# Optimization experiments

Hardware: AMD Instinct MI355X
Metric: run time of the kernel (lower is better)

## Reference

```python
import jax, jax.numpy as jnp
import numpy as np

ALPHA = 0.5
TEMPORAL_UNIT = 0
B, T, D = 8, 1024, 320
TIME_MAX = 10_000_000


def setup_inputs() -> dict:
    key = jax.random.key(0)
    k1, k2, k3 = jax.random.split(key, 3)
    z1 = jax.random.normal(k1, (B, T, D), dtype=jnp.float32)
    z2 = jax.random.normal(k2, (B, T, D), dtype=jnp.float32)
    event_time = jnp.sort(
        jax.random.randint(k3, (B, T), 0, TIME_MAX, dtype=jnp.int32), axis=-1
    )
    return {"z1": z1, "z2": z2, "event_time": event_time}


def _neg_logsoftmax_offdiag(sim):
    # tril(sim,-1)[...,:-1] + triu(sim,1)[...,1:]  -> (.., N, N-1), then -log_softmax
    logits = jnp.tril(sim, -1)[..., :-1] + jnp.triu(sim, 1)[..., 1:]
    return -jax.nn.log_softmax(logits, axis=-1)


def _instance_loss(z1, z2):
    b, t = z1.shape[0], z1.shape[1]
    if b == 1:
        return jnp.float32(0.0)
    z = jnp.concatenate([z1, z2], axis=0).transpose(1, 0, 2)  # (T, 2B, D)
    sim = jnp.einsum('tid,tjd->tij', z, z)                    # (T, 2B, 2B)
    logits = _neg_logsoftmax_offdiag(sim)                     # (T, 2B, 2B-1)
    i = jnp.arange(b)
    return (logits[:, i, b + i - 1].mean() + logits[:, b + i, i].mean()) / 2


def _temporal_loss(z1, z2):
    t = z1.shape[1]
    if t == 1:
        return jnp.float32(0.0)
    z = jnp.concatenate([z1, z2], axis=1)                     # (B, 2T, D)
    sim = jnp.einsum('bid,bjd->bij', z, z)                    # (B, 2T, 2T)
    logits = _neg_logsoftmax_offdiag(sim)                     # (B, 2T, 2T-1)
    ti = jnp.arange(t)
    return (logits[:, ti, t + ti - 1].mean() + logits[:, t + ti, ti].mean()) / 2


def _pool_and_filter(z, time):
    # max_pool1d(kernel=2, stride=1) over time axis
    bsz, seq_len, dim = z.shape
    pooled = jnp.maximum(z[:, :-1], z[:, 1:])                  # (B, T-1, D)
    pooled_time = (time[:, :-1] + time[:, 1:]) // 2            # (B, T-1)
    deltas = jnp.diff(time, axis=-1)                           # (B, T-1)
    indices = jnp.argsort(deltas, axis=-1)                     # permutation of 0..T-2
    mask = indices < seq_len // 2                              # exactly T//2 Trues/row
    tm1 = seq_len - 1
    ar = jnp.arange(tm1)
    # stable in-order selection of masked positions: masked keys keep their index,
    # unmasked keys are pushed past the end; sort + take first T//2
    sel = jnp.sort(jnp.where(mask, ar, ar + tm1), axis=-1)[:, : seq_len // 2]
    pooled = jnp.take_along_axis(pooled, sel[:, :, None], axis=1)
    pooled_time = jnp.take_along_axis(pooled_time, sel, axis=1)
    return pooled, pooled_time


def _hier_loss(z1, z2, time, alpha=ALPHA, temporal_unit=TEMPORAL_UNIT):
    loss = jnp.float32(0.0)
    d = 0
    while z1.shape[1] > 1:  # static Python loop over hierarchy levels
        if alpha != 0:
            loss = loss + alpha * _instance_loss(z1, z2)
        if d >= temporal_unit and (1 - alpha) != 0:
            loss = loss + (1 - alpha) * _temporal_loss(z1, z2)
        d += 1
        z1, _ = _pool_and_filter(z1, time)
        z2, time = _pool_and_filter(z2, time)
    if z1.shape[1] == 1:
        if alpha != 0:
            loss = loss + alpha * _instance_loss(z1, z2)
        d += 1
    return loss / d


def reference(z1, z2, event_time):
    return _hier_loss(z1, z2, event_time)
```

## Files before the change

### kernel.cpp

```cpp
#include <hip/hip_runtime.h>
#include <cstdint>
#include <cstddef>

#define D_DIM 320
#define NEGINF (-1e30f)

typedef __attribute__((ext_vector_type(8))) short bf16x8_t;
typedef __attribute__((ext_vector_type(4))) float f32x4_t;
typedef __attribute__((ext_vector_type(16))) float f32x16_t;

struct Tab {
  int T[11], S[11], zoff[11], wsoff[11];
  int tileStart[12], instStart[12], rstart[12];
  float scale[11];
  int totTemp, totInst, totr;
};

__device__ __forceinline__ float bf2f(unsigned short u) {
  union { unsigned int i; float f; } v; v.i = ((unsigned int)u) << 16; return v.f;
}
__device__ __forceinline__ unsigned short f2bf(float f) {
  union { float f; unsigned int i; } u; u.f = f;
  unsigned int b = u.i + 0x7FFFu + ((u.i >> 16) & 1u);
  return (unsigned short)(b >> 16);
}

__device__ __forceinline__ const unsigned short* zrowb(
    const unsigned short* __restrict__ z1, const unsigned short* __restrict__ z2,
    int b, int T, int r) {
  return (r < T) ? (z1 + ((size_t)b * T + r) * D_DIM)
                 : (z2 + ((size_t)b * T + (r - T)) * D_DIM);
}

#define GLOAD_LDS16(SRC, DST)                                                   \
  __builtin_amdgcn_global_load_lds(                                             \
      (const __attribute__((address_space(1))) void*)(SRC),                     \
      (__attribute__((address_space(3))) void*)(DST), 16, 0, 0)

#define BUF1 8192
#define BUF2 16384

#define STAGE(koff, bufofs)                                                     \
    do {                                                                        \
      GLOAD_LDS16(gA0 + (koff), dA0 + (bufofs));                                \
      GLOAD_LDS16(gA1 + (koff), dA1 + (bufofs));                                \
      GLOAD_LDS16(gB0 + (koff), dB0 + (bufofs));                                \
      GLOAD_LDS16(gB1 + (koff), dB1 + (bufofs));                                \
    } while (0)

#define PHASE3(k, bo, bo2, VM, DO_PF)                                           \
    do {                                                                        \
      asm volatile("s_waitcnt vmcnt(" #VM ")" ::: "memory");                    \
      __builtin_amdgcn_s_barrier();                                             \
      if (DO_PF) STAGE((k + 2) * 32, bo2);                                      \
      bf16x8_t af[4], bfr[4];                                                   \
      _Pragma("unroll")                                                         \
      for (int at = 0; at < 4; ++at)                                            \
        af[at] = *(const bf16x8_t*)(vA + (bo) + at * 128);                      \
      _Pragma("unroll")                                                         \
      for (int ct = 0; ct < 4; ++ct)                                            \
        bfr[ct] = *(const bf16x8_t*)(vB + (bo) + ct * 128);                     \
      asm volatile("s_waitcnt lgkmcnt(0)" ::: "memory");                        \
      __builtin_amdgcn_sched_barrier(0);                                        \
      __builtin_amdgcn_s_setprio(1);                                            \
      _Pragma("unroll")                                                         \
      for (int ct = 0; ct < 4; ++ct)                                            \
        _Pragma("unroll")                                                       \
        for (int at = 0; at < 4; ++at)                                          \
          acc[at][ct] = __builtin_amdgcn_mfma_f32_16x16x32_bf16(                \
              af[at], bfr[ct], acc[at][ct], 0, 0, 0);                           \
      __builtin_amdgcn_s_setprio(0);                                            \
    } while (0)

__device__ __forceinline__ void tile_body(
    unsigned char* smem, int tid,
    const unsigned short* zz1, const unsigned short* zz2,
    int b, int T, int S, int rb, int sg,
    float* wm, float* wv, float* wp) {
  int N = 2 * T;
  int row0 = rb * 128, col0 = sg * 128;
  int w = tid >> 6, lane = tid & 63;
  int lq = lane >> 4, lr = lane & 15;
  int wr = w >> 1, wc = w & 1;

  unsigned short* lds = (unsigned short*)smem;

  int ra0 = row0 + lane;        if (ra0 > N - 1) ra0 = N - 1;
  int ra1 = row0 + 64 + lane;   if (ra1 > N - 1) ra1 = N - 1;
  int ca0 = col0 + lane;        if (ca0 > N - 1) ca0 = N - 1;
  int ca1 = col0 + 64 + lane;   if (ca1 > N - 1) ca1 = N - 1;
  const unsigned short* gA0 = zrowb(zz1, zz2, b, T, ra0) + w * 8;
  const unsigned short* gA1 = zrowb(zz1, zz2, b, T, ra1) + w * 8;
  const unsigned short* gB0 = zrowb(zz1, zz2, b, T, ca0) + w * 8;
  const unsigned short* gB1 = zrowb(zz1, zz2, b, T, ca1) + w * 8;
  unsigned short* dA0 = &lds[((w) * 128 + lane) * 8];
  unsigned short* dA1 = &lds[((w) * 128 + 64 + lane) * 8];
  unsigned short* dB0 = &lds[((4 + w) * 128 + lane) * 8];
  unsigned short* dB1 = &lds[((4 + w) * 128 + 64 + lane) * 8];

  f32x4_t acc[4][4];
#pragma unroll
  for (int at = 0; at < 4; ++at)
#pragma unroll
    for (int ct = 0; ct < 4; ++ct) acc[at][ct] = (f32x4_t)(0.f);

  const unsigned short* vA = &lds[((lq) * 128 + wr * 64 + lr) * 8];
  const unsigned short* vB = &lds[((4 + lq) * 128 + wc * 64 + lr) * 8];

  STAGE(0, 0);
  STAGE(32, BUF1);
  PHASE3(0, 0,    BUF2, 4, 1);
  PHASE3(1, BUF1, 0,    4, 1);
  PHASE3(2, BUF2, BUF1, 4, 1);
  PHASE3(3, 0,    BUF2, 4, 1);
  PHASE3(4, BUF1, 0,    4, 1);
  PHASE3(5, BUF2, BUF1, 4, 1);
  PHASE3(6, 0,    BUF2, 4, 1);
  PHASE3(7, BUF1, 0,    4, 1);
  PHASE3(8, BUF2, 0,    4, 0);
  PHASE3(9, 0,    0,    0, 0);
  __builtin_amdgcn_s_barrier();

  float (*mS)[128] = (float(*)[128])(smem);
  float (*sS)[128] = (float(*)[128])(smem + 1024);
  float (*mC)[128] = (float(*)[128])(smem + 2048);
  float (*sC)[128] = (float(*)[128])(smem + 3072);

#pragma unroll
  for (int at = 0; at < 4; ++at) {
#pragma unroll
    for (int rg = 0; rg < 4; ++rg) {
      int rloc = wr * 64 + at * 16 + lq * 4 + rg;
      int rglob = row0 + rloc;
      int posr = (rglob < T) ? rglob + T : rglob - T;
      float v[4];
#pragma unroll
      for (int ct = 0; ct < 4; ++ct) {
        int cg = col0 + wc * 64 + ct * 16 + lr;
        float val = acc[at][ct][rg];
        if (rglob < N && cg == posr) {
          wp[b * N + rglob] = val;
          wp[b * N + cg] = val;
        }
        v[ct] = (cg < N && cg != rglob) ? val : NEGINF;
      }
      float m = fmaxf(fmaxf(v[0], v[1]), fmaxf(v[2], v[3]));
#pragma unroll
      for (int o = 1; o < 16; o <<= 1) m = fmaxf(m, __shfl_xor(m, o));
      float sv = __expf(v[0] - m) + __expf(v[1] - m) +
                 __expf(v[2] - m) + __expf(v[3] - m);
#pragma unroll
      for (int o = 1; o < 16; o <<= 1) sv += __shfl_xor(sv, o);
      if (lr == 0) { mS[wc][rloc] = m; sS[wc][rloc] = sv; }
    }
  }
  if (rb != sg) {
#pragma unroll
    for (int ct = 0; ct < 4; ++ct) {
      float m = NEGINF;
#pragma unroll
      for (int at = 0; at < 4; ++at)
#pragma unroll
        for (int rg = 0; rg < 4; ++rg) m = fmaxf(m, acc[at][ct][rg]);
      m = fmaxf(m, __shfl_xor(m, 16));
      m = fmaxf(m, __shfl_xor(m, 32));
      float s = 0.f;
#pragma unroll
      for (int at = 0; at < 4; ++at)
#pragma unroll
        for (int rg = 0; rg < 4; ++rg) s += __expf(acc[at][ct][rg] - m);
      s += __shfl_xor(s, 16);
      s += __shfl_xor(s, 32);
      if (lq == 0) {
        mC[wr][wc * 64 + ct * 16 + lr] = m;
        sC[wr][wc * 64 + ct * 16 + lr] = s;
      }
    }
  }
  __syncthreads();

  if (tid < 128) {
    int rglob = row0 + tid;
    if (rglob < N) {
      float m0 = mS[0][tid], m1 = mS[1][tid];
      float m = fmaxf(m0, m1);
      float sv = sS[0][tid] * __expf(m0 - m) + sS[1][tid] * __expf(m1 - m);
      int idx = (b * S + sg) * N + rglob;
      wm[idx] = m;
      wv[idx] = sv;
    }
    if (rb != sg) {
      float m0 = mC[0][tid], m1 = mC[1][tid];
      float m = fmaxf(m0, m1);
      float sv = sC[0][tid] * __expf(m0 - m) + sC[1][tid] * __expf(m1 - m);
      int idx = (b * S + rb) * N + col0 + tid;
      wm[idx] = m;
      wv[idx] = sv;
    }
  }
}

__device__ __forceinline__ float inst_wave(
    const unsigned short* zz1, const unsigned short* zz2, int T, int t, int lane) {
  int lq = lane >> 4, lr = lane & 15;
  const unsigned short* zr = (lr < 8)
      ? zz1 + ((size_t)lr * T + t) * D_DIM
      : zz2 + ((size_t)(lr - 8) * T + t) * D_DIM;
  zr += lq * 8;
  f32x4_t c = (f32x4_t)(0.f);
#pragma unroll
  for (int k = 0; k < 10; ++k) {
    bf16x8_t a = *(const bf16x8_t*)(zr + k * 32);
    c = __builtin_amdgcn_mfma_f32_16x16x32_bf16(a, a, c, 0, 0, 0);
  }
  float lsum = 0.f;
#pragma unroll
  for (int rg = 0; rg < 4; ++rg) {
    int rrow = lq * 4 + rg;
    float v = c[rg];
    float x = (lr != rrow) ? v : NEGINF;
    float m = x;
#pragma unroll
    for (int o = 1; o < 16; o <<= 1) m = fmaxf(m, __shfl_xor(m, o));
    float s = __expf(x - m);
#pragma unroll
    for (int o = 1; o < 16; o <<= 1) s += __shfl_xor(s, o);
    int pos = (rrow < 8) ? rrow + 8 : rrow - 8;
    if (lr == pos) lsum += m + __logf(s) - v;
  }
#pragma unroll
  for (int o = 1; o < 64; o <<= 1) lsum += __shfl_xor(lsum, o);
  return lsum;
}

__global__ __launch_bounds__(256) void convert_kernel(
    const float* __restrict__ i1, const float* __restrict__ i2,
    unsigned short* __restrict__ o1, unsigned short* __restrict__ o2,
    int n4, float* __restrict__ out, int outn) {
  int i = blockIdx.x * 256 + threadIdx.x;
  if (i < outn) out[i] = 0.f;
  int stride = gridDim.x * 256;
  for (int j = i; j < n4; j += stride) {
    float4 v = ((const float4*)i1)[j];
    ushort4 r;
    r.x = f2bf(v.x); r.y = f2bf(v.y); r.z = f2bf(v.z); r.w = f2bf(v.w);
    ((ushort4*)o1)[j] = r;
    float4 u = ((const float4*)i2)[j];
    ushort4 q;
    q.x = f2bf(u.x); q.y = f2bf(u.y); q.z = f2bf(u.z); q.w = f2bf(u.w);
    ((ushort4*)o2)[j] = q;
  }
}

__global__ __launch_bounds__(256, 3) void work0_kernel(
    const int* __restrict__ time0,
    const unsigned short* __restrict__ z1, const unsigned short* __restrict__ z2,
    float* __restrict__ wsm, float* __restrict__ wss, float* __restrict__ wpos,
    float* __restrict__ wsInst,
    int* __restrict__ SET0, int* __restrict__ L0LEN,
    int* __restrict__ SET5, int* __restrict__ L5LEN) {
  __shared__ __align__(16) unsigned char smem[49152];
  int bx = blockIdx.x;
  int tid = threadIdx.x;

  if (bx < 8) {
    int b = bx;
    int lane = tid & 63, wid = tid >> 6;
    int* tcur = (int*)smem;
    unsigned* hist = (unsigned*)(smem + 4096);
    unsigned short* cum = (unsigned short*)(smem + 12288);
    unsigned long long* arr = (unsigned long long*)(smem + 16384);
    int* sortedIdx = (int*)(smem + 24576);
    int* tnew = (int*)(smem + 28672);
    int* srcK = (int*)(smem + 30720);
    int* setA = (int*)(smem + 32768);
    int* setB = (int*)(smem + 36864);
    int* lenA = (int*)(smem + 40960);
    int* lenB = (int*)(smem + 45056);
    unsigned* minW = (unsigned*)(smem + 47104);
    unsigned* maxW = (unsigned*)(smem + 47168);
    unsigned* wsum = (unsigned*)(smem + 47232);
    int* wcnt = (int*)(smem + 47296);

#pragma unroll
    for (int i = 0; i < 4; ++i) {
      int e = tid + 256 * i;
      tcur[e] = time0[b * 1024 + e];
      setA[e] = e;
      lenA[e] = 1;
    }
    __syncthreads();

    int pp = 0;
    for (int lvl = 1; lvl <= 10; ++lvl) {
      int T = 2048 >> lvl;
      int n = T - 1, half = T >> 1;
      bool act[4];
      int dd[4];
      unsigned bkey[4];
      unsigned mn = 0xFFFFFFFFu, mx = 0u;
#pragma unroll
      for (int i = 0; i < 4; ++i) {
        int e = tid + 256 * i;
        act[i] = e < n;
        dd[i] = 0; bkey[i] = 0;
        if (act[i]) {
          dd[i] = tcur[e + 1] - tcur[e];
          bkey[i] = __float_as_uint((float)dd[i]);
          mn = mn < bkey[i] ? mn : bkey[i];
          mx = mx > bkey[i] ? mx : bkey[i];
        }
        hist[e] = 0;
        hist[e + 1024] = 0;
      }
#pragma unroll
      for (int o = 1; o < 64; o <<= 1) {
        unsigned m2 = (unsigned)__shfl_xor((int)mn, o);
        unsigned x2 = (unsigned)__shfl_xor((int)mx, o);
        mn = mn < m2 ? mn : m2;
        mx = mx > x2 ? mx : x2;
      }
      if (lane == 0) { minW[wid] = mn; maxW[wid] = mx; }
      __syncthreads();

      unsigned bmin = 0xFFFFFFFFu, bmax = 0;
#pragma unroll
      for (int i = 0; i < 4; ++i) {
        bmin = bmin < minW[i] ? bmin : minW[i];
        bmax = bmax > maxW[i] ? bmax : maxW[i];
      }
      unsigned long long range = (unsigned long long)(bmax - bmin) + 1;
      unsigned long long scl = (2048ULL << 30) / range;
      int bkt[4]; unsigned av[4];
#pragma unroll
      for (int i = 0; i < 4; ++i) {
        if (act[i]) {
          int bk = (int)(((unsigned long long)(bkey[i] - bmin) * scl) >> 30);
          bkt[i] = bk > 2047 ? 2047 : bk;
          av[i] = atomicAdd(&hist[bkt[i]], 1u);
        }
      }
      __syncthreads();

      {
        unsigned lv[8];
        unsigned s = 0;
#pragma unroll
        for (int j = 0; j < 8; ++j) { lv[j] = hist[8 * tid + j]; s += lv[j]; }
        unsigned inc = s;
#pragma unroll
        for (int o = 1; o < 64; o <<= 1) {
          unsigned t = (unsigned)__shfl_up((int)inc, o);
          if (lane >= o) inc += t;
        }
        if (lane == 63) wsum[wid] = inc;
        __syncthreads();
        unsigned wpre = 0;
        for (int j = 0; j < wid; ++j) wpre += wsum[j];
        unsigned ex = wpre + inc - s;
#pragma unroll
        for (int j = 0; j < 8; ++j) { cum[8 * tid + j] = (unsigned short)ex; ex += lv[j]; }
      }
      __syncthreads();

      unsigned long long key[4];
      int base[4], occ[4];
#pragma unroll
      for (int i = 0; i < 4; ++i) {
        base[i] = 0; occ[i] = 0;
        if (act[i]) {
          key[i] = ((unsigned long long)(unsigned)dd[i] << 10) |
                   (unsigned)(tid + 256 * i);
          base[i] = (int)cum[bkt[i]];
          arr[base[i] + av[i]] = key[i];
        }
      }
      __syncthreads();

      int cnt[4] = {0, 0, 0, 0};
      int mocc = 0;
#pragma unroll
      for (int i = 0; i < 4; ++i) {
        if (act[i]) {
          occ[i] = (int)hist[bkt[i]];
          mocc = occ[i] > mocc ? occ[i] : mocc;
        }
      }
      for (int j = 0; j < mocc; ++j) {
#pragma unroll
        for (int i = 0; i < 4; ++i)
          if (j < occ[i]) cnt[i] += (arr[base[i] + j] < key[i]) ? 1 : 0;
      }
#pragma unroll
      for (int i = 0; i < 4; ++i)
        if (act[i]) sortedIdx[base[i] + cnt[i]] = tid + 256 * i;
      __syncthreads();

      bool msk[4]; int rw[4];
#pragma unroll
      for (int i = 0; i < 4; ++i) {
        int k = tid + 256 * i;
        msk[i] = (k < n) && (sortedIdx[k] < half);
        unsigned long long bal = __ballot(msk[i]);
        rw[i] = __popcll(bal & ((1ull << lane) - 1ull));
        if (lane == 0) wcnt[i * 4 + wid] = (int)__popcll(bal);
      }
      __syncthreads();
#pragma unroll
      for (int i = 0; i < 4; ++i) {
        if (msk[i]) {
          int seg = i * 4 + wid;
          int pre = 0;
          for (int j = 0; j < seg; ++j) pre += wcnt[j];
          int rr = pre + rw[i];
          int k = tid + 256 * i;
          srcK[rr] = k;
          tnew[rr] = (tcur[k] + tcur[k + 1]) >> 1;
        }
      }
      __syncthreads();

      if (lvl == 6) {
        int* sp = pp ? setB : setA;
        int* lp = pp ? lenB : lenA;
        if (tid < 32) { sp[tid] = tid; lp[tid] = 1; }
        __syncthreads();
      }
      {
        int ll = (lvl <= 5) ? lvl : (lvl - 5);
        int* sp = pp ? setB : setA;
        int* lp = pp ? lenB : lenA;
        int* sc = pp ? setA : setB;
        int* lc = pp ? lenA : lenB;
        int *gset, *glen;
        if (lvl <= 5) {
          gset = SET0 + b * 5120 + (lvl - 1) * 1024;
          glen = L0LEN + b * 992 + (1024 - (1024 >> (lvl - 1)));
        } else {
          gset = SET5 + b * 160 + (lvl - 6) * 32;
          glen = L5LEN + b * 32 + (32 - (32 >> (lvl - 6)));
        }
        int tmax = half << ll;
#pragma unroll
        for (int i = 0; i < 4; ++i) {
          int s = tid + 256 * i;
          if (s < tmax) {
            int j = s >> ll, e2 = s & ((1 << ll) - 1);
            int k = srcK[j];
            int la = lp[k], lb2 = lp[k + 1];
            int v = -1;
            int sh = ll - 1;
            if (e2 < la) v = sp[(k << sh) + e2];
            else if (e2 < la + lb2) v = sp[((k + 1) << sh) + (e2 - la)];
            if (e2 == 0) { lc[j] = la + lb2; glen[j] = la + lb2; }
            if (v >= 0) { sc[s] = v; gset[s] = v; }
          }
        }
        __syncthreads();
        pp ^= 1;
      }
#pragma unroll
      for (int i = 0; i < 4; ++i) {
        int j = tid + 256 * i;
        if (j < half) tcur[j] = tnew[j];
      }
      __syncthreads();
    }
  } else if (bx < 8 + 1088) {
    const int T = 1024, S = 16;
    int local = bx - 8;
    int b = local % 8;
    int pr = local / 8;
    int rb = 0, tt = pr;
    while (tt >= S - rb) { tt -= S - rb; ++rb; }
    int sg = rb + tt;
    tile_body(smem, tid, z1, z2, b, T, S, rb, sg, wsm, wss, wpos);
  } else {
    int iw = (bx - 1096) * 4 + (tid >> 6);
    float lsum = inst_wave(z1, z2, 1024, iw, tid & 63);
    if ((tid & 63) == 0) wsInst[iw] = lsum * (1.0f / 360448.0f);
  }
}

__global__ __launch_bounds__(256) void mat1_kernel(
    unsigned short* __restrict__ z1, unsigned short* __restrict__ z2,
    const int* __restrict__ SET0, const int* __restrict__ L0LEN) {
  int g = blockIdx.x * 256 + threadIdx.x;
  int c = g % 40;
  int t2 = g / 40;
  int rr = t2 % 992;
  int bzi = t2 / 992;
  int b = bzi & 7;
  unsigned short* z = (bzi >> 3) ? z2 : z1;
  int l, j, off0;
  if (rr < 512)      { l = 1; j = rr;       off0 = 0; }
  else if (rr < 768) { l = 2; j = rr - 512; off0 = 512; }
  else if (rr < 896) { l = 3; j = rr - 768; off0 = 768; }
  else if (rr < 960) { l = 4; j = rr - 896; off0 = 896; }
  else               { l = 5; j = rr - 960; off0 = 960; }
  int len = L0LEN[b * 992 + off0 + j];
  const int* st = SET0 + b * 5120 + (l - 1) * 1024 + (j << l);
  const unsigned short* src = z + (size_t)b * 1024 * D_DIM;
  int cc = c * 8;
  bf16x8_t mx = *(const bf16x8_t*)(src + (size_t)st[0] * D_DIM + cc);
  for (int e = 1; e < len; ++e) {
    bf16x8_t a = *(const bf16x8_t*)(src + (size_t)st[e] * D_DIM + cc);
#pragma unroll
    for (int q = 0; q < 8; ++q)
      mx[q] = (bf2f((unsigned short)mx[q]) >= bf2f((unsigned short)a[q])) ? mx[q] : a[q];
  }
  size_t zo = (size_t)2560 * (2048 - (2048 >> l));
  int Tl = 1024 >> l;
  *(bf16x8_t*)(z + zo + ((size_t)b * Tl + j) * D_DIM + cc) = mx;
}

__global__ __launch_bounds__(256, 3) void work45_kernel(
    unsigned short* __restrict__ z1, unsigned short* __restrict__ z2,
    const int* __restrict__ SET5, const int* __restrict__ L5LEN,
    float* __restrict__ wsm, float* __restrict__ wss, float* __restrict__ wpos,
    float* __restrict__ wsInst, Tab tab) {
  __shared__ __align__(16) unsigned char smem[49152];
  int bx = blockIdx.x;
  int tid = threadIdx.x;

  if (bx < 408) {
    int g = tab.tileStart[1] + bx;
    int l = 1;
    while (g >= tab.tileStart[l + 1]) ++l;
    int T = tab.T[l], S = tab.S[l];
    int local = g - tab.tileStart[l];
    int npl = (S * (S + 1)) >> 1;
    int nid = (local % 8) * npl + local / 8;
    int b = nid / npl;
    int pr = nid % npl;
    int rb = 0, tt = pr;
    while (tt >= S - rb) { tt -= S - rb; ++rb; }
    int sg = rb + tt;
    tile_body(smem, tid, z1 + tab.zoff[l], z2 + tab.zoff[l], b, T, S, rb, sg,
              wsm + tab.wsoff[l], wss + tab.wsoff[l], wpos + tab.rstart[l]);
  } else if (bx < 486) {
    int g = (bx - 408) * 256 + tid;
    if (g >= 2 * 8 * 31 * 40) return;
    int c = g % 40;
    int t2 = g / 40;
    int rr = t2 % 31;
    int bzi = t2 / 31;
    int b = bzi & 7;
    unsigned short* z = (bzi >> 3) ? z2 : z1;
    int l, j, off5;
    if (rr < 16)      { l = 6;  j = rr;      off5 = 0; }
    else if (rr < 24) { l = 7;  j = rr - 16; off5 = 16; }
    else if (rr < 28) { l = 8;  j = rr - 24; off5 = 24; }
    else if (rr < 30) { l = 9;  j = rr - 28; off5 = 28; }
    else              { l = 10; j = rr - 30; off5 = 30; }
    int len = L5LEN[b * 32 + off5 + j];
    const int* st = SET5 + b * 160 + (l - 6) * 32 + (j << (l - 5));
    const unsigned short* src = z + (size_t)2560 * (2048 - 64) + (size_t)b * 32 * D_DIM;
    int cc = c * 8;
    bf16x8_t mx = *(const bf16x8_t*)(src + (size_t)st[0] * D_DIM + cc);
    for (int e = 1; e < len; ++e) {
      bf16x8_t a = *(const bf16x8_t*)(src + (size_t)st[e] * D_DIM + cc);
#pragma unroll
      for (int q = 0; q < 8; ++q)
        mx[q] = (bf2f((unsigned short)mx[q]) >= bf2f((unsigned short)a[q])) ? mx[q] : a[q];
    }
    size_t zo = (size_t)2560 * (2048 - (2048 >> l));
    int Tl = 1024 >> l;
    *(bf16x8_t*)(z + zo + ((size_t)b * Tl + j) * D_DIM + cc) = mx;
  } else {
    int iw = 1024 + (bx - 486) * 4 + (tid >> 6);
    if (iw < 2016) {
      int l = 1;
      while (iw >= tab.instStart[l + 1]) ++l;
      int t = iw - tab.instStart[l];
      float lsum = inst_wave(z1 + tab.zoff[l], z2 + tab.zoff[l], tab.T[l], t,
                             tid & 63);
      if ((tid & 63) == 0) wsInst[iw] = lsum * tab.scale[l];
    }
  }
}

__global__ __launch_bounds__(256) void final_kernel(
    const unsigned short* __restrict__ z1, const unsigned short* __restrict__ z2,
    const float* __restrict__ wsm, const float* __restrict__ wss,
    const float* __restrict__ wpos,
    const float* __restrict__ wsInst, float* __restrict__ out, Tab tab,
    int nc) {
  int bx = blockIdx.x;
  int tid = threadIdx.x;

  if (bx < nc) {
    int g = bx * 256 + tid;
    float loss = 0.f;
    if (g < tab.totr) {
      int l = 0;
      while (g >= tab.rstart[l + 1]) ++l;
      int row = g - tab.rstart[l];
      int T = tab.T[l], N = 2 * T, S = tab.S[l];
      int b = row / N, r = row % N;
      const float* wm = wsm + tab.wsoff[l];
      const float* wv = wss + tab.wsoff[l];
      float m = NEGINF;
      for (int s = 0; s < S; ++s) m = fmaxf(m, wm[(b * S + s) * N + r]);
      float sv = 0.f;
      for (int s = 0; s < S; ++s) {
        int idx = (b * S + s) * N + r;
        sv += wv[idx] * __expf(wm[idx] - m);
      }
      float dot = wpos[tab.rstart[l] + b * N + r];
      loss = (m + logf(sv) - dot) * tab.scale[l];
    } else if (g < tab.totr + 2016) {
      loss = wsInst[g - tab.totr];
    }
    float v = loss;
#pragma unroll
    for (int o = 1; o < 64; o <<= 1) v += __shfl_xor(v, o);
    __shared__ float part[4];
    int w = tid >> 6;
    if ((tid & 63) == 0) part[w] = v;
    __syncthreads();
    if (tid == 0)
      atomicAdd(out, part[0] + part[1] + part[2] + part[3]);
  } else if (bx < nc + 8) {
    int widx = (bx - nc) * 4 + (tid >> 6);
    int l = 6 + (widx >> 3), b = widx & 7;
    int T = tab.T[l], N = 2 * T;
    const unsigned short* zz1 = z1 + tab.zoff[l];
    const unsigned short* zz2 = z2 + tab.zoff[l];
    int lane = tid & 63;
    int col = lane & 31, h = lane >> 5;
    int rl = (col < N) ? col : 0;
    const unsigned short* rowp = (rl < T)
        ? zz1 + ((size_t)b * T + rl) * D_DIM
        : zz2 + ((size_t)b * T + (rl - T)) * D_DIM;
    rowp += h * 8;
    f32x16_t acc = (f32x16_t)(0.f);
#pragma unroll
    for (int m2 = 0; m2 < 20; ++m2) {
      bf16x8_t a = *(const bf16x8_t*)(rowp + m2 * 16);
      acc = __builtin_amdgcn_mfma_f32_32x32x16_bf16(a, a, acc, 0, 0, 0);
    }
    float lsum = 0.f;
#pragma unroll
    for (int rg = 0; rg < 16; ++rg) {
      int row = (rg & 3) + 8 * (rg >> 2) + 4 * h;
      float x = acc[rg];
      float xm = (col < N && row < N && col != row) ? x : NEGINF;
      float m = xm;
#pragma unroll
      for (int o = 1; o < 32; o <<= 1) m = fmaxf(m, __shfl_xor(m, o));
      float s = __expf(xm - m);
#pragma unroll
      for (int o = 1; o < 32; o <<= 1) s += __shfl_xor(s, o);
      int pos = (row < T) ? row + T : row - T;
      if (row < N && col == pos) lsum += m + __logf(s) - x;
    }
#pragma unroll
    for (int o = 1; o < 64; o <<= 1) lsum += __shfl_xor(lsum, o);
    if (lane == 0) atomicAdd(out, lsum * tab.scale[l]);
  } else {
    int widx = (bx - nc - 8) * 4 + (tid >> 6);
    if (widx < 31) {
      int iw = 2016 + widx;
      int l = 6;
      while (iw >= tab.instStart[l + 1]) ++l;
      int t = iw - tab.instStart[l];
      float lsum = inst_wave(z1 + tab.zoff[l], z2 + tab.zoff[l], tab.T[l], t,
                             tid & 63);
      if ((tid & 63) == 0) atomicAdd(out, lsum * tab.scale[l]);
    }
  }
}

extern "C" void kernel_launch(void* const* d_in, const int* in_sizes, int n_in,
                              void* d_out, int out_size, void* d_ws, size_t ws_size,
                              hipStream_t stream) {
  const float* z1_in = (const float*)d_in[0];
  const float* z2_in = (const float*)d_in[1];
  const int* time_in = (const int*)d_in[2];
  float* out = (float*)d_out;

  Tab tab;
  int zo = 0, wso = 0, ts = 0, is = 0, rs = 0;
  for (int l = 0; l < 11; ++l) {
    int T = 1024 >> l, N = 2 * T;
    int S = (N >= 128) ? N / 128 : 1;
    tab.T[l] = T;
    tab.S[l] = S;
    tab.zoff[l] = zo;
    tab.scale[l] = 1.0f / (352.0f * (float)T);
    tab.tileStart[l] = ts;
    tab.instStart[l] = is;
    tab.wsoff[l] = (T > 1) ? wso : 0;
    tab.rstart[l] = rs;
    if (T > 1) {
      ts += 8 * ((S * (S + 1)) >> 1);
      wso += 8 * S * N;
      if (l <= 5) rs += 8 * N;
    }
    is += T;
    zo += 8 * T * D_DIM;
  }
  tab.tileStart[11] = ts;
  tab.instStart[11] = is;
  for (int l = 6; l <= 11; ++l) tab.rstart[l] = rs;
  tab.totTemp = ts;
  tab.totInst = is;
  tab.totr = rs;

  char* w = (char*)d_ws;
  unsigned short* z1s = (unsigned short*)w; w += (size_t)zo * 2;
  unsigned short* z2s = (unsigned short*)w; w += (size_t)zo * 2;
  float* wsm = (float*)w; w += (size_t)wso * sizeof(float);
  float* wss = (float*)w; w += (size_t)wso * sizeof(float);
  float* wpos = (float*)w; w += (size_t)rs * sizeof(float);
  float* wsInst = (float*)w; w += (size_t)is * sizeof(float);
  int* SET0 = (int*)w; w += (size_t)8 * 5120 * sizeof(int);
  int* L0LEN = (int*)w; w += (size_t)8 * 992 * sizeof(int);
  int* SET5 = (int*)w; w += (size_t)8 * 160 * sizeof(int);
  int* L5LEN = (int*)w; w += (size_t)8 * 32 * sizeof(int);

  int n0 = 8 * 1024 * D_DIM;
  convert_kernel<<<2048, 256, 0, stream>>>(z1_in, z2_in, z1s, z2s, n0 / 4,
                                           out, out_size);
  work0_kernel<<<8 + 1088 + 256, 256, 0, stream>>>(
      time_in, z1s, z2s, wsm, wss, wpos, wsInst, SET0, L0LEN, SET5, L5LEN);
  mat1_kernel<<<2480, 256, 0, stream>>>(z1s, z2s, SET0, L0LEN);
  work45_kernel<<<408 + 78 + 248, 256, 0, stream>>>(
      z1s, z2s, SET5, L5LEN, wsm, wss, wpos, wsInst, tab);
  int nc = (tab.totr + 2016 + 255) / 256;
  final_kernel<<<nc + 16, 256, 0, stream>>>(z1s, z2s, wsm, wss, wpos, wsInst,
                                            out, tab, nc);
}
```

Measured before the change: 104.0 us.

## Move set-building into conversion kernel and merge pooling into work0

The per-batch pooling/selection logic (8 blocks) now runs alongside the fp32-to-bf16 conversion in a single prep kernel, and the level-1..5 pooled-row materialization (former mat1 kernel) is merged into work0 with the level-0 tiles and instance waves. This cuts one launch and lets the serial 8-block argsort overlap the bandwidth-bound conversion instead of stalling the level-0 tiles. The bucketed histogram sort is replaced by a plain O(n^2) rank count over shared memory, which drops the histogram and scan stages but does more comparisons per thread. It also shrinks that path's shared memory. Merging mat1 into work0 is only safe if no level-0 tile or instance wave reads the level-1..5 rows it writes, since those blocks now run concurrently.

Measured after the change: 169.4 us. 62.9% more time.

```diff
diff --git a/kernel.cpp b/kernel.cpp
--- a/kernel.cpp
+++ b/kernel.cpp
@@ -233,33 +233,14 @@
   return lsum;
 }
 
-__global__ __launch_bounds__(256) void convert_kernel(
+__global__ __launch_bounds__(256) void prep_kernel(
+    const int* __restrict__ time0,
     const float* __restrict__ i1, const float* __restrict__ i2,
     unsigned short* __restrict__ o1, unsigned short* __restrict__ o2,
-    int n4, float* __restrict__ out, int outn) {
-  int i = blockIdx.x * 256 + threadIdx.x;
-  if (i < outn) out[i] = 0.f;
-  int stride = gridDim.x * 256;
-  for (int j = i; j < n4; j += stride) {
-    float4 v = ((const float4*)i1)[j];
-    ushort4 r;
-    r.x = f2bf(v.x); r.y = f2bf(v.y); r.z = f2bf(v.z); r.w = f2bf(v.w);
-    ((ushort4*)o1)[j] = r;
-    float4 u = ((const float4*)i2)[j];
-    ushort4 q;
-    q.x = f2bf(u.x); q.y = f2bf(u.y); q.z = f2bf(u.z); q.w = f2bf(u.w);
-    ((ushort4*)o2)[j] = q;
-  }
-}
-
-__global__ __launch_bounds__(256, 3) void work0_kernel(
-    const int* __restrict__ time0,
-    const unsigned short* __restrict__ z1, const unsigned short* __restrict__ z2,
-    float* __restrict__ wsm, float* __restrict__ wss, float* __restrict__ wpos,
-    float* __restrict__ wsInst,
+    int n4, float* __restrict__ out, int outn, int nconv,
     int* __restrict__ SET0, int* __restrict__ L0LEN,
     int* __restrict__ SET5, int* __restrict__ L5LEN) {
-  __shared__ __align__(16) unsigned char smem[49152];
+  __shared__ __align__(16) unsigned char smem[36928];
   int bx = blockIdx.x;
   int tid = threadIdx.x;
 
@@ -267,20 +248,15 @@
     int b = bx;
     int lane = tid & 63, wid = tid >> 6;
     int* tcur = (int*)smem;
-    unsigned* hist = (unsigned*)(smem + 4096);
-    unsigned short* cum = (unsigned short*)(smem + 12288);
-    unsigned long long* arr = (unsigned long long*)(smem + 16384);
-    int* sortedIdx = (int*)(smem + 24576);
-    int* tnew = (int*)(smem + 28672);
-    int* srcK = (int*)(smem + 30720);
-    int* setA = (int*)(smem + 32768);
-    int* setB = (int*)(smem + 36864);
-    int* lenA = (int*)(smem + 40960);
-    int* lenB = (int*)(smem + 45056);
-    unsigned* minW = (unsigned*)(smem + 47104);
-    unsigned* maxW = (unsigned*)(smem + 47168);
-    unsigned* wsum = (unsigned*)(smem + 47232);
-    int* wcnt = (int*)(smem + 47296);
+    unsigned long long* arr = (unsigned long long*)(smem + 4096);
+    int* sortedIdx = (int*)(smem + 12288);
+    int* tnew = (int*)(smem + 16384);
+    int* srcK = (int*)(smem + 18432);
+    int* setA = (int*)(smem + 20480);
+    int* setB = (int*)(smem + 24576);
+    int* lenA = (int*)(smem + 28672);
+    int* lenB = (int*)(smem + 32768);
+    int* wcnt = (int*)(smem + 34816);
 
 #pragma unroll
     for (int i = 0; i < 4; ++i) {
@@ -296,104 +272,38 @@
       int T = 2048 >> lvl;
       int n = T - 1, half = T >> 1;
       bool act[4];
-      int dd[4];
-      unsigned bkey[4];
-      unsigned mn = 0xFFFFFFFFu, mx = 0u;
+      unsigned long long key[4];
 #pragma unroll
       for (int i = 0; i < 4; ++i) {
         int e = tid + 256 * i;
         act[i] = e < n;
-        dd[i] = 0; bkey[i] = 0;
+        key[i] = ~0ULL;
         if (act[i]) {
-          dd[i] = tcur[e + 1] - tcur[e];
-          bkey[i] = __float_as_uint((float)dd[i]);
-          mn = mn < bkey[i] ? mn : bkey[i];
-          mx = mx > bkey[i] ? mx : bkey[i];
+          unsigned d = (unsigned)(tcur[e + 1] - tcur[e]);
+          key[i] = ((unsigned long long)d << 10) | (unsigned)e;
+          arr[e] = key[i];
         }
-        hist[e] = 0;
-        hist[e + 1024] = 0;
-      }
-#pragma unroll
-      for (int o = 1; o < 64; o <<= 1) {
-        unsigned m2 = (unsigned)__shfl_xor((int)mn, o);
-        unsigned x2 = (unsigned)__shfl_xor((int)mx, o);
-        mn = mn < m2 ? mn : m2;
-        mx = mx > x2 ? mx : x2;
-      }
-      if (lane == 0) { minW[wid] = mn; maxW[wid] = mx; }
+      }
       __syncthreads();
 
-      unsigned bmin = 0xFFFFFFFFu, bmax = 0;
-#pragma unroll
-      for (int i = 0; i < 4; ++i) {
-        bmin = bmin < minW[i] ? bmin : minW[i];
-        bmax = bmax > maxW[i] ? bmax : maxW[i];
-      }
-      unsigned long long range = (unsigned long long)(bmax - bmin) + 1;
-      unsigned long long scl = (2048ULL << 30) / range;
-      int bkt[4]; unsigned av[4];
-#pragma unroll
-      for (int i = 0; i < 4; ++i) {
-        if (act[i]) {
-          int bk = (int)(((unsigned long long)(bkey[i] - bmin) * scl) >> 30);
-          bkt[i] = bk > 2047 ? 2047 : bk;
-          av[i] = atomicAdd(&hist[bkt[i]], 1u);
-        }
-      }
-      __syncthreads();
-
-      {
-        unsigned lv[8];
-        unsigned s = 0;
-#pragma unroll
-        for (int j = 0; j < 8; ++j) { lv[j] = hist[8 * tid + j]; s += lv[j]; }
-        unsigned inc = s;
-#pragma unroll
-        for (int o = 1; o < 64; o <<= 1) {
-          unsigned t = (unsigned)__shfl_up((int)inc, o);
-          if (lane >= o) inc += t;
-        }
-        if (lane == 63) wsum[wid] = inc;
-        __syncthreads();
-        unsigned wpre = 0;
-        for (int j = 0; j < wid; ++j) wpre += wsum[j];
-        unsigned ex = wpre + inc - s;
-#pragma unroll
-        for (int j = 0; j < 8; ++j) { cum[8 * tid + j] = (unsigned short)ex; ex += lv[j]; }
-      }
-      __syncthreads();
-
-      unsigned long long key[4];
-      int base[4], occ[4];
-#pragma unroll
-      for (int i = 0; i < 4; ++i) {
-        base[i] = 0; occ[i] = 0;
-        if (act[i]) {
-          key[i] = ((unsigned long long)(unsigned)dd[i] << 10) |
-                   (unsigned)(tid + 256 * i);
-          base[i] = (int)cum[bkt[i]];
-          arr[base[i] + av[i]] = key[i];
-        }
-      }
-      __syncthreads();
-
       int cnt[4] = {0, 0, 0, 0};
-      int mocc = 0;
-#pragma unroll
-      for (int i = 0; i < 4; ++i) {
-        if (act[i]) {
-          occ[i] = (int)hist[bkt[i]];
-          mocc = occ[i] > mocc ? occ[i] : mocc;
-        }
-      }
-      for (int j = 0; j < mocc; ++j) {
+      int j = 0;
+      for (; j + 4 <= n; j += 4) {
+        unsigned long long k0 = arr[j], k1 = arr[j + 1],
+                           k2 = arr[j + 2], k3 = arr[j + 3];
 #pragma unroll
         for (int i = 0; i < 4; ++i)
-          if (j < occ[i]) cnt[i] += (arr[base[i] + j] < key[i]) ? 1 : 0;
+          cnt[i] += (int)(k0 < key[i]) + (int)(k1 < key[i]) +
+                    (int)(k2 < key[i]) + (int)(k3 < key[i]);
+      }
+      for (; j < n; ++j) {
+        unsigned long long kj = arr[j];
+#pragma unroll
+        for (int i = 0; i < 4; ++i) cnt[i] += (int)(kj < key[i]);
       }
 #pragma unroll
       for (int i = 0; i < 4; ++i)
-        if (act[i]) sortedIdx[base[i] + cnt[i]] = tid + 256 * i;
+        if (act[i]) sortedIdx[cnt[i]] = tid + 256 * i;
       __syncthreads();
 
       bool msk[4]; int rw[4];
@@ -411,7 +321,7 @@
         if (msk[i]) {
           int seg = i * 4 + wid;
           int pre = 0;
-          for (int j = 0; j < seg; ++j) pre += wcnt[j];
+          for (int q = 0; q < seg; ++q) pre += wcnt[q];
           int rr = pre + rw[i];
           int k = tid + 256 * i;
           srcK[rr] = k;
@@ -442,17 +352,17 @@
         }
         int tmax = half << ll;
 #pragma unroll
-        for (int i = 0; i < 4; ++i) {
+      for (int i = 0; i < 4; ++i) {
           int s = tid + 256 * i;
           if (s < tmax) {
-            int j = s >> ll, e2 = s & ((1 << ll) - 1);
-            int k = srcK[j];
+            int jj = s >> ll, e2 = s & ((1 << ll) - 1);
+            int k = srcK[jj];
             int la = lp[k], lb2 = lp[k + 1];
             int v = -1;
             int sh = ll - 1;
             if (e2 < la) v = sp[(k << sh) + e2];
             else if (e2 < la + lb2) v = sp[((k + 1) << sh) + (e2 - la)];
-            if (e2 == 0) { lc[j] = la + lb2; glen[j] = la + lb2; }
+            if (e2 == 0) { lc[jj] = la + lb2; glen[jj] = la + lb2; }
             if (v >= 0) { sc[s] = v; gset[s] = v; }
           }
         }
@@ -461,57 +371,78 @@
       }
 #pragma unroll
       for (int i = 0; i < 4; ++i) {
-        int j = tid + 256 * i;
-        if (j < half) tcur[j] = tnew[j];
+        int jj = tid + 256 * i;
+        if (jj < half) tcur[jj] = tnew[jj];
       }
       __syncthreads();
     }
-  } else if (bx < 8 + 1088) {
+  } else {
+    int i = (bx - 8) * 256 + tid;
+    if (i < outn) out[i] = 0.f;
+    int stride = nconv * 256;
+    for (int j = i; j < n4; j += stride) {
+      float4 v = ((const float4*)i1)[j];
+      ushort4 r;
+      r.x = f2bf(v.x); r.y = f2bf(v.y); r.z = f2bf(v.z); r.w = f2bf(v.w);
+      ((ushort4*)o1)[j] = r;
+      float4 u = ((const float4*)i2)[j];
+      ushort4 q;
+      q.x = f2bf(u.x); q.y = f2bf(u.y); q.z = f2bf(u.z); q.w = f2bf(u.w);
+      ((ushort4*)o2)[j] = q;
+    }
+  }
+}
+
+__global__ __launch_bounds__(256, 3) void work0_kernel(
+    unsigned short* __restrict__ z1, unsigned short* __restrict__ z2,
+    float* __restrict__ wsm, float* __restrict__ wss, float* __restrict__ wpos,
+    float* __restrict__ wsInst,
+    const int* __restrict__ SET0, const int* __restrict__ L0LEN) {
+  __shared__ __align__(16) unsigned char smem[49152];
+  int bx = blockIdx.x;
+  int tid = threadIdx.x;
+
+  if (bx < 1088) {
     const int T = 1024, S = 16;
-    int local = bx - 8;
-    int b = local % 8;
-    int pr = local / 8;
+    int b = bx % 8;
+    int pr = bx / 8;
     int rb = 0, tt = pr;
     while (tt >= S - rb) { tt -= S - rb; ++rb; }
     int sg = rb + tt;
     tile_body(smem, tid, z1, z2, b, T, S, rb, sg, wsm, wss, wpos);
+  } else if (bx < 1088 + 2480) {
+    int g = (bx - 1088) * 256 + tid;
+    int c = g % 40;
+    int t2 = g / 40;
+    int rr = t2 % 992;
+    int bzi = t2 / 992;
+    int b = bzi & 7;
+    unsigned short* z = (bzi >> 3) ? z2 : z1;
+    int l, j, off0;
+    if (rr < 512)      { l = 1; j = rr;       off0 = 0; }
+    else if (rr < 768) { l = 2; j = rr - 512; off0 = 512; }
+    else if (rr < 896) { l = 3; j = rr - 768; off0 = 768; }
+    else if (rr < 960) { l = 4; j = rr - 896; off0 = 896; }
+    else               { l = 5; j = rr - 960; off0 = 960; }
+    int len = L0LEN[b * 992 + off0 + j];
+    const int* st = SET0 + b * 5120 + (l - 1) * 1024 + (j << l);
+    const unsigned short* src = z + (size_t)b * 1024 * D_DIM;
+    int cc = c * 8;
+    bf16x8_t mx = *(const bf16x8_t*)(src + (size_t)st[0] * D_DIM + cc);
+    for (int e = 1; e < len; ++e) {
+      bf16x8_t a = *(const bf16x8_t*)(src + (size_t)st[e] * D_DIM + cc);
+#pragma unroll
+      for (int q = 0; q < 8; ++q)
+        mx[q] = (bf2f((unsigned short)mx[q]) >= bf2f((unsigned short)a[q])) ? mx[q] : a[q];
+    }
+    size_t zo = (size_t)2560 * (2048 - (2048 >> l));
+    int Tl = 1024 >> l;
+    *(bf16x8_t*)(z + zo + ((size_t)b * Tl + j) * D_DIM + cc) = mx;
   } else {
-    int iw = (bx - 1096) * 4 + (tid >> 6);
+    int iw = (bx - 3568) * 4 + (tid >> 6);
     float lsum = inst_wave(z1, z2, 1024, iw, tid & 63);
     if ((tid & 63) == 0) wsInst[iw] = lsum * (1.0f / 360448.0f);
   }
-}
-
-__global__ __launch_bounds__(256) void mat1_kernel(
-    unsigned short* __restrict__ z1, unsigned short* __restrict__ z2,
-    const int* __restrict__ SET0, const int* __restrict__ L0LEN) {
-  int g = blockIdx.x * 256 + threadIdx.x;
-  int c = g % 40;
-  int t2 = g / 40;
-  int rr = t2 % 992;
-  int bzi = t2 / 992;
-  int b = bzi & 7;
-  unsigned short* z = (bzi >> 3) ? z2 : z1;
-  int l, j, off0;
-  if (rr < 512)      { l = 1; j = rr;       off0 = 0; }
-  else if (rr < 768) { l = 2; j = rr - 512; off0 = 512; }
-  else if (rr < 896) { l = 3; j = rr - 768; off0 = 768; }
-  else if (rr < 960) { l = 4; j = rr - 896; off0 = 896; }
-  else               { l = 5; j = rr - 960; off0 = 960; }
-  int len = L0LEN[b * 992 + off0 + j];
-  const int* st = SET0 + b * 5120 + (l - 1) * 1024 + (j << l);
-  const unsigned short* src = z + (size_t)b * 1024 * D_DIM;
-  int cc = c * 8;
-  bf16x8_t mx = *(const bf16x8_t*)(src + (size_t)st[0] * D_DIM + cc);
-  for (int e = 1; e < len; ++e) {
-    bf16x8_t a = *(const bf16x8_t*)(src + (size_t)st[e] * D_DIM + cc);
-#pragma unroll
-    for (int q = 0; q < 8; ++q)
-      mx[q] = (bf2f((unsigned short)mx[q]) >= bf2f((unsigned short)a[q])) ? mx[q] : a[q];
-  }
-  size_t zo = (size_t)2560 * (2048 - (2048 >> l));
-  int Tl = 1024 >> l;
-  *(bf16x8_t*)(z + zo + ((size_t)b * Tl + j) * D_DIM + cc) = mx;
 }
 
 __global__ __launch_bounds__(256, 3) void work45_kernel(
@@ -721,11 +652,12 @@
   int* L5LEN = (int*)w; w += (size_t)8 * 32 * sizeof(int);
 
   int n0 = 8 * 1024 * D_DIM;
-  convert_kernel<<<2048, 256, 0, stream>>>(z1_in, z2_in, z1s, z2s, n0 / 4,
-                                           out, out_size);
-  work0_kernel<<<8 + 1088 + 256, 256, 0, stream>>>(
-      time_in, z1s, z2s, wsm, wss, wpos, wsInst, SET0, L0LEN, SET5, L5LEN);
-  mat1_kernel<<<2480, 256, 0, stream>>>(z1s, z2s, SET0, L0LEN);
+  int nconv = 2040;
+  prep_kernel<<<8 + nconv, 256, 0, stream>>>(time_in, z1_in, z2_in, z1s, z2s,
+                                             n0 / 4, out, out_size, nconv,
+                                             SET0, L0LEN, SET5, L5LEN);
+  work0_kernel<<<1088 + 2480 + 256, 256, 0, stream>>>(
+      z1s, z2s, wsm, wss, wpos, wsInst, SET0, L0LEN);
   work45_kernel<<<408 + 78 + 248, 256, 0, stream>>>(
       z1s, z2s, SET5, L5LEN, wsm, wss, wpos, wsInst, tab);
   int nc = (tab.totr + 2016 + 255) / 256;
```
